# Kernel optimization log

Hardware: AMD Instinct MI355X
Metric: run time of the kernel (lower is better)

## Reference

```python
import jax, jax.numpy as jnp
import numpy as np

NEG = -9e8

def _leaky(x):
    return jax.nn.leaky_relu(x, 0.01)

def _gru(x, h, wih, whh, bih, bhh):
    # torch.nn.GRUCell math
    gi = x @ wih.T + bih
    gh = h @ whh.T + bhh
    ir, iz, inn = jnp.split(gi, 3, axis=-1)
    hr, hz, hn = jnp.split(gh, 3, axis=-1)
    r = jax.nn.sigmoid(ir + hr)
    z = jax.nn.sigmoid(iz + hz)
    n = jnp.tanh(inn + r * hn)
    return (1.0 - z) * n + z * h

def _gather(feat, idx):
    # feat [B,S,F], idx [B,S,K] -> [B,S,K,F]; -1 wraps to last row, masked later (same as torch)
    return jax.vmap(lambda f, i: f[i])(feat, idx)

def setup_inputs() -> dict:
    key = jax.random.key(0)
    ks = jax.random.split(key, 32)
    B, S, K, F_in, E, R = 32, 512, 21, 26, 256, 3
    amino_list = jax.random.uniform(ks[0], (B, S, F_in), dtype=jnp.float32)
    idx = jax.random.randint(ks[1], (B, S, K), 0, S, dtype=jnp.int32)
    pad = jax.random.uniform(ks[2], (B, S, K)) < 0.3
    amino_degree_list = jnp.where(pad, jnp.int32(-1), idx)
    # variable sequence lengths for mask
    lens = jax.random.randint(ks[3], (B,), S // 2, S + 1)
    amino_mask = (jnp.arange(S)[None, :] < lens[:, None]).astype(jnp.float32)
    s = 0.05
    d = dict(
        amino_list=amino_list,
        amino_degree_list=amino_degree_list,
        amino_mask=amino_mask,
        emb_W=jax.random.normal(ks[4], (E, F_in)) * s,
        emb_b=jax.random.normal(ks[5], (E,)) * s,
        neigh_W=jax.random.normal(ks[6], (E, F_in)) * s,
        neigh_b=jax.random.normal(ks[7], (E,)) * s,
        align_W=jax.random.normal(ks[8], (R, 1, 2 * E)) * s,
        align_b=jax.random.normal(ks[9], (R, 1)) * s,
        attend_W=jax.random.normal(ks[10], (R, E, E)) * s,
        attend_b=jax.random.normal(ks[11], (R, E)) * s,
        gru_wih=jax.random.normal(ks[12], (R, 3 * E, E)) * s,
        gru_whh=jax.random.normal(ks[13], (R, 3 * E, E)) * s,
        gru_bih=jax.random.normal(ks[14], (R, 3 * E)) * s,
        gru_bhh=jax.random.normal(ks[15], (R, 3 * E)) * s,
        seq_align_W=jax.random.normal(ks[16], (1, 2 * E)) * s,
        seq_align_b=jax.random.normal(ks[17], (1,)) * s,
        seq_attend_W=jax.random.normal(ks[18], (E, E)) * s,
        seq_attend_b=jax.random.normal(ks[19], (E,)) * s,
        sgru_wih=jax.random.normal(ks[20], (3 * E, E)) * s,
        sgru_whh=jax.random.normal(ks[21], (3 * E, E)) * s,
        sgru_bih=jax.random.normal(ks[22], (3 * E,)) * s,
        sgru_bhh=jax.random.normal(ks[23], (3 * E,)) * s,
    )
    return d

RADIUS = 3
T_STEPS = 2

def reference(amino_list, amino_degree_list, amino_mask,
              emb_W, emb_b, neigh_W, neigh_b,
              align_W, align_b, attend_W, attend_b,
              gru_wih, gru_whh, gru_bih, gru_bhh,
              seq_align_W, seq_align_b, seq_attend_W, seq_attend_b,
              sgru_wih, sgru_whh, sgru_bih, sgru_bhh):
    B, S, _ = amino_list.shape
    E = emb_W.shape[0]
    K = amino_degree_list.shape[-1]

    mask3 = amino_mask[:, :, None]                       # [B,S,1]
    amino_feature = _leaky(amino_list @ emb_W.T + emb_b)  # [B,S,E]

    attend_mask = (amino_degree_list != -1).astype(jnp.float32)[..., None]   # [B,S,K,1]
    softmax_mask = jnp.where(amino_degree_list == -1, NEG, 0.0)[..., None]   # [B,S,K,1]

    # first radius step: neighbors from raw one-hot features via neighbor_fc
    neighbor = _gather(amino_list, amino_degree_list)                 # [B,S,K,F_in]
    neighbor_feature = _leaky(neighbor @ neigh_W.T + neigh_b)         # [B,S,K,E]

    h = amino_feature.reshape(B * S, E)
    activated = None
    for d in range(RADIUS):
        if d == 0:
            nbr = neighbor_feature
            cur = amino_feature
        else:
            nbr = _gather(activated, amino_degree_list)               # [B,S,K,E]
            cur = activated
        cur_exp = jnp.broadcast_to(cur[:, :, None, :], (B, S, K, E))
        feat_align = jnp.concatenate([cur_exp, nbr], axis=-1)         # [B,S,K,2E]
        score = _leaky(feat_align @ align_W[d].T + align_b[d]) + softmax_mask
        attw = jax.nn.softmax(score, axis=-2) * attend_mask           # [B,S,K,1]
        nbr_t = nbr @ attend_W[d].T + attend_b[d]                     # [B,S,K,E]
        context = jax.nn.elu(jnp.sum(attw * nbr_t, axis=-2))          # [B,S,E]
        h = _gru(context.reshape(B * S, E), h, gru_wih[d], gru_whh[d], gru_bih[d], gru_bhh[d])
        activated = jax.nn.relu(h.reshape(B, S, E))

    seq_feature = jnp.sum(activated * mask3, axis=-2)                 # [B,E]
    act_mol = jax.nn.relu(seq_feature)
    seq_softmax_mask = jnp.where(mask3 == 0.0, NEG, 0.0)              # [B,S,1]

    act_seq = act_mol
    for _ in range(T_STEPS):
        mol_exp = jnp.broadcast_to(act_mol[:, None, :], (B, S, E))
        sa = jnp.concatenate([mol_exp, activated], axis=-1)           # [B,S,2E]
        score = _leaky(sa @ seq_align_W.T + seq_align_b) + seq_softmax_mask
        w = jax.nn.softmax(score, axis=-2) * mask3                    # [B,S,1]
        feat_t = activated @ seq_attend_W.T + seq_attend_b            # [B,S,E]
        seq_context = jax.nn.elu(jnp.sum(w * feat_t, axis=-2))        # [B,E]
        seq_feature = _gru(seq_context, seq_feature, sgru_wih, sgru_whh, sgru_bih, sgru_bhh)
        act_seq = jax.nn.relu(seq_feature)
    return act_seq
```

## Files before the change

### kernel.cpp

```cpp
#include <hip/hip_runtime.h>
#include <hip/hip_bf16.h>
#include <math.h>


#define NEGC (-9.0e8f)

typedef __attribute__((ext_vector_type(8))) short bf16x8;
typedef __attribute__((ext_vector_type(4))) float f32x4;

__device__ __forceinline__ ushort f2bf(float x) {
    union { float f; unsigned u; } v; v.f = x;
    unsigned r = v.u + 0x7FFF + ((v.u >> 16) & 1);
    return (ushort)(r >> 16);
}
__device__ __forceinline__ float bf2f(ushort u) {
    union { unsigned u; float f; } v; v.u = ((unsigned)u) << 16;
    return v.f;
}
__device__ __forceinline__ float sigm_fast(float x) {
    return 1.f / (1.f + __expf(-x));
}
__device__ __forceinline__ float tanh_fast(float x) {
    return 1.f - 2.f / (__expf(2.f * x) + 1.f);
}
__device__ __forceinline__ float elu_fast(float x) {
    return x > 0.f ? x : (__expf(x) - 1.f);
}

typedef const __attribute__((address_space(1))) void gvoid_t;
typedef __attribute__((address_space(3))) void lvoid_t;

__global__ __launch_bounds__(256) void cvt3_kernel(
    const float* __restrict__ s0, ushort* __restrict__ d0, int n0,
    const float* __restrict__ s1, ushort* __restrict__ d1, int n1,
    const float* __restrict__ s2, ushort* __restrict__ d2, int n2)
{
    int i = blockIdx.x * 256 + threadIdx.x;
    const float* s; ushort* dst; int l;
    if (i < n0) { s = s0; dst = d0; l = i; }
    else if (i < n0 + n1) { s = s1; dst = d1; l = i - n0; }
    else if (i < n0 + n1 + n2) { s = s2; dst = d2; l = i - n0 - n1; }
    else return;
    float4 v = *reinterpret_cast<const float4*>(s + (size_t)l * 4);
    ushort4 o; o.x = f2bf(v.x); o.y = f2bf(v.y); o.z = f2bf(v.z); o.w = f2bf(v.w);
    *reinterpret_cast<ushort4*>(dst + (size_t)l * 4) = o;
}

__global__ __launch_bounds__(256) void gemm_dual_kernel(
    const ushort* __restrict__ A0, const ushort* __restrict__ W0,
    const float* __restrict__ b0, ushort* __restrict__ C0, int n0t,
    int K,
    const float* __restrict__ dw1, const float* __restrict__ dw2,
    float* __restrict__ dout1, float* __restrict__ dout2)
{
    __shared__ __align__(16) short As[128 * 32];
    __shared__ __align__(16) short Bs[128 * 32];
    int nwg = gridDim.x;
    int q = nwg >> 3;
    int flat = blockIdx.x;
    int sw = (flat & 7) * q + (flat >> 3);
    int bmi = sw / n0t, bni = sw - bmi * n0t;
    const ushort* A = A0; const ushort* W = W0; const float* bias = b0;
    ushort* C = C0; int N = n0t << 7; int bn = bni << 7;
    int bm = bmi << 7;

    int tid = threadIdx.x;
    int lane = tid & 63;
    int w = tid >> 6;
    int wr = w >> 1, wc = w & 1;
    bool dots = (dout1 != nullptr) && (bni == 0);

    f32x4 acc[4][4];
#pragma unroll
    for (int m = 0; m < 4; ++m)
#pragma unroll
        for (int n = 0; n < 4; ++n) acc[m][n] = (f32x4){0.f, 0.f, 0.f, 0.f};
    float p1 = 0.f, p2 = 0.f;

    for (int k0 = 0; k0 < K; k0 += 32) {
#pragma unroll
        for (int i = 0; i < 2; ++i) {
            int e = w * 1024 + i * 512 + lane * 8;
            int r = e >> 5, c = e & 31;
            const ushort* ga = A + (size_t)(bm + r) * K + (k0 + c);
            const ushort* gw = W + (size_t)(bn + r) * K + (k0 + c);
            __builtin_amdgcn_global_load_lds((gvoid_t*)ga, (lvoid_t*)&As[w * 1024 + i * 512], 16, 0, 0);
            __builtin_amdgcn_global_load_lds((gvoid_t*)gw, (lvoid_t*)&Bs[w * 1024 + i * 512], 16, 0, 0);
        }
        __syncthreads();
        bf16x8 af[4], bw[4];
        int ra = wr * 64 + (lane & 15);
        int rb = wc * 64 + (lane & 15);
        int kc = (lane >> 4) * 8;
#pragma unroll
        for (int m = 0; m < 4; ++m)
            af[m] = *reinterpret_cast<const bf16x8*>(&As[(ra + m * 16) * 32 + kc]);
#pragma unroll
        for (int n = 0; n < 4; ++n)
            bw[n] = *reinterpret_cast<const bf16x8*>(&Bs[(rb + n * 16) * 32 + kc]);
#pragma unroll
        for (int m = 0; m < 4; ++m)
#pragma unroll
            for (int n = 0; n < 4; ++n)
                acc[m][n] = __builtin_amdgcn_mfma_f32_16x16x32_bf16(af[m], bw[n], acc[m][n], 0, 0, 0);
        if (dots) {
            int drow = tid >> 1, kh = (tid & 1) << 4;
            const short* ar = &As[drow * 32 + kh];
#pragma unroll
            for (int c = 0; c < 16; ++c) {
                float av = bf2f((ushort)ar[c]);
                p1 = fmaf(av, dw1[k0 + kh + c], p1);
                p2 = fmaf(av, dw2[k0 + kh + c], p2);
            }
        }
        __syncthreads();
    }

    if (dots) {
        p1 += __shfl_xor(p1, 1);
        p2 += __shfl_xor(p2, 1);
        if ((tid & 1) == 0) {
            dout1[bm + (tid >> 1)] = p1;
            dout2[bm + (tid >> 1)] = p2;
        }
    }

    int cr0 = bm + wr * 64 + ((lane >> 4) * 4);
    int cc0 = bn + wc * 64 + (lane & 15);
#pragma unroll
    for (int n = 0; n < 4; ++n) {
        int col = cc0 + n * 16;
        float bv = bias[col];
#pragma unroll
        for (int m = 0; m < 4; ++m) {
            int row0 = cr0 + m * 16;
#pragma unroll
            for (int j = 0; j < 4; ++j) {
                float v = acc[m][n][j] + bv;
                C[(size_t)(row0 + j) * N + col] = f2bf(v);
            }
        }
    }
}

template<bool TAIL>
__global__ __launch_bounds__(256) void gru_fused_kernel(
    const ushort* __restrict__ ctx, const ushort* __restrict__ wih,
    const float* __restrict__ bih, const ushort* __restrict__ whh,
    const float* __restrict__ bhh,
    const ushort* __restrict__ h_in, ushort* __restrict__ h_out,
    ushort* __restrict__ act_bf,
    const float* __restrict__ mask, float* __restrict__ pool_part,
    const float* __restrict__ dsw, float* __restrict__ scor_part, int BS)
{
    __shared__ __align__(16) short lds[16384];
    int flat = blockIdx.x;
    int sw = (flat & 7) * 128 + (flat >> 3);
    int bmi = sw >> 2, ct = sw & 3;
    int bm = bmi << 6;
    int tid = threadIdx.x;
    int lane = tid & 63;
    int w = tid >> 6;
    int wr = w >> 1, wc = w & 1;

    f32x4 acc[6][2][2];
#pragma unroll
    for (int qq = 0; qq < 6; ++qq)
#pragma unroll
        for (int m = 0; m < 2; ++m)
#pragma unroll
            for (int n = 0; n < 2; ++n) acc[qq][m][n] = (f32x4){0.f, 0.f, 0.f, 0.f};

    int srow = tid >> 2, scol = (tid & 3) << 3;
    int ldst = (tid & 0xC0) * 8;
    for (int k0 = 0; k0 < 256; k0 += 32) {
        {
            const ushort* s0 = ctx  + (size_t)(bm + srow) * 256 + k0 + scol;
            const ushort* s1 = h_in + (size_t)(bm + srow) * 256 + k0 + scol;
            __builtin_amdgcn_global_load_lds((gvoid_t*)s0, (lvoid_t*)&lds[ldst], 16, 0, 0);
            __builtin_amdgcn_global_load_lds((gvoid_t*)s1, (lvoid_t*)&lds[2048 + ldst], 16, 0, 0);
#pragma unroll
            for (int qq = 0; qq < 6; ++qq) {
                const ushort* wb = (qq < 3) ? wih : whh;
                int slice = (qq < 3) ? qq : qq - 3;
                const ushort* sv = wb + (size_t)(slice * 256 + ct * 64 + srow) * 256 + k0 + scol;
                __builtin_amdgcn_global_load_lds((gvoid_t*)sv,
                    (lvoid_t*)&lds[(2 + qq) * 2048 + ldst], 16, 0, 0);
            }
        }
        __syncthreads();
        int rl = lane & 15;
        int kc = (lane >> 4) * 8;
        bf16x8 a_c[2], a_h[2];
#pragma unroll
        for (int m = 0; m < 2; ++m) {
            a_c[m] = *reinterpret_cast<const bf16x8*>(&lds[(wr * 32 + m * 16 + rl) * 32 + kc]);
            a_h[m] = *reinterpret_cast<const bf16x8*>(&lds[2048 + (wr * 32 + m * 16 + rl) * 32 + kc]);
        }
#pragma unroll
        for (int qq = 0; qq < 6; ++qq) {
            bf16x8 bw[2];
#pragma unroll
            for (int n = 0; n < 2; ++n)
                bw[n] = *reinterpret_cast<const bf16x8*>(
                    &lds[(2 + qq) * 2048 + (wc * 32 + n * 16 + rl) * 32 + kc]);
#pragma unroll
            for (int m = 0; m < 2; ++m)
#pragma unroll
                for (int n = 0; n < 2; ++n)
                    acc[qq][m][n] = __builtin_amdgcn_mfma_f32_16x16x32_bf16(
                        (qq < 3) ? a_c[m] : a_h[m], bw[n], acc[qq][m][n], 0, 0, 0);
        }
        __syncthreads();
    }

    int rl = lane & 15;
    int r0 = (lane >> 4) * 4;
    float mv[2][4];
    float dswv[2];
    if (TAIL) {
        int b_ = bm >> 9;
        int sbase = bm & 511;
#pragma unroll
        for (int m = 0; m < 2; ++m)
#pragma unroll
            for (int j = 0; j < 4; ++j)
                mv[m][j] = mask[b_ * 512 + sbase + wr * 32 + m * 16 + r0 + j];
#pragma unroll
        for (int n = 0; n < 2; ++n)
            dswv[n] = dsw[ct * 64 + wc * 32 + n * 16 + rl];
    }
    float pm[2] = {0.f, 0.f};
    float ps[2][4] = {{0.f, 0.f, 0.f, 0.f}, {0.f, 0.f, 0.f, 0.f}};

#pragma unroll
    for (int n = 0; n < 2; ++n) {
        int col = ct * 64 + wc * 32 + n * 16 + rl;
        float bir = bih[col], biz = bih[256 + col], bin = bih[512 + col];
        float bhr = bhh[col], bhz = bhh[256 + col], bhn = bhh[512 + col];
#pragma unroll
        for (int m = 0; m < 2; ++m) {
            int row0 = bm + wr * 32 + m * 16 + r0;
#pragma unroll
            for (int j = 0; j < 4; ++j) {
                size_t idx = (size_t)(row0 + j) * 256 + col;
                float r = sigm_fast(acc[0][m][n][j] + bir + acc[3][m][n][j] + bhr);
                float z = sigm_fast(acc[1][m][n][j] + biz + acc[4][m][n][j] + bhz);
                float nn = tanh_fast(acc[2][m][n][j] + bin + r * (acc[5][m][n][j] + bhn));
                float hold = bf2f(h_in[idx]);
                float hh = (1.f - z) * nn + z * hold;
                h_out[idx] = f2bf(hh);
                float a = fmaxf(hh, 0.f);
                act_bf[idx] = f2bf(a);
                if (TAIL) {
                    pm[n] = fmaf(a, mv[m][j], pm[n]);
                    ps[m][j] = fmaf(a, dswv[n], ps[m][j]);
                }
            }
        }
    }

    if (TAIL) {
#pragma unroll
        for (int n = 0; n < 2; ++n) {
            float p = pm[n];
            p += __shfl_xor(p, 16);
            p += __shfl_xor(p, 32);
            if (lane < 16) {
                int b_ = bm >> 9;
                int sc = ((bm & 511) >> 5) + wr;
                int col = ct * 64 + wc * 32 + n * 16 + rl;
                pool_part[((size_t)b_ * 16 + sc) * 256 + col] = p;
            }
        }
#pragma unroll
        for (int m = 0; m < 2; ++m)
#pragma unroll
            for (int j = 0; j < 4; ++j) {
                float p = ps[m][j];
                p += __shfl_xor(p, 1);
                p += __shfl_xor(p, 2);
                p += __shfl_xor(p, 4);
                p += __shfl_xor(p, 8);
                if (rl == 0) {
                    int row = bm + wr * 32 + m * 16 + r0 + j;
                    scor_part[(size_t)(ct * 2 + wc) * BS + row] = p;
                }
            }
    }
}

__global__ __launch_bounds__(256) void embed_kernel(
    const float* __restrict__ amino, const float* __restrict__ embW,
    const float* __restrict__ embB, const float* __restrict__ neighW,
    const float* __restrict__ neighB, const float* __restrict__ alignW,
    ushort* __restrict__ h_bf, ushort* __restrict__ nf_bf,
    float* __restrict__ ca, float* __restrict__ cb)
{
    const int FIN = 26, FPAD = 28, ROWS = 64;
    __shared__ __align__(16) float xs[ROWS][FPAD];
    __shared__ float red1[ROWS][4];
    __shared__ float red2[ROWS][4];
    int tid = threadIdx.x;
    int lane = tid & 63, wv = tid >> 6;
    float wE[FPAD], wN[FPAD];
#pragma unroll
    for (int f = 0; f < FIN; ++f) {
        wE[f] = embW[tid * FIN + f];
        wN[f] = neighW[tid * FIN + f];
    }
    wE[26] = wE[27] = wN[26] = wN[27] = 0.f;
    float b1 = embB[tid], b2 = neighB[tid];
    float w1t = alignW[tid], w2t = alignW[256 + tid];
    int row0 = blockIdx.x * ROWS;
    for (int idx = tid; idx < ROWS * FPAD; idx += 256) {
        int r = idx / FPAD, f = idx - r * FPAD;
        xs[r][f] = (f < FIN) ? amino[(size_t)(row0 + r) * FIN + f] : 0.f;
    }
    __syncthreads();
    for (int r = 0; r < ROWS; ++r) {
        const float4* x4 = reinterpret_cast<const float4*>(xs[r]);
        float a = b1, c = b2;
#pragma unroll
        for (int q = 0; q < 7; ++q) {
            float4 x = x4[q];
            a = fmaf(x.x, wE[4 * q], a);     c = fmaf(x.x, wN[4 * q], c);
            a = fmaf(x.y, wE[4 * q + 1], a); c = fmaf(x.y, wN[4 * q + 1], c);
            a = fmaf(x.z, wE[4 * q + 2], a); c = fmaf(x.z, wN[4 * q + 2], c);
            a = fmaf(x.w, wE[4 * q + 3], a); c = fmaf(x.w, wN[4 * q + 3], c);
        }
        a = a > 0.f ? a : 0.01f * a;
        c = c > 0.f ? c : 0.01f * c;
        size_t idx = (size_t)(row0 + r) * 256 + tid;
        h_bf[idx] = f2bf(a);
        nf_bf[idx] = f2bf(c);
        float p1 = a * w1t, p2 = c * w2t;
#pragma unroll
        for (int off = 32; off > 0; off >>= 1) {
            p1 += __shfl_down(p1, off);
            p2 += __shfl_down(p2, off);
        }
        if (lane == 0) { red1[r][wv] = p1; red2[r][wv] = p2; }
    }
    __syncthreads();
    if (tid < ROWS)
        ca[row0 + tid] = red1[tid][0] + red1[tid][1] + red1[tid][2] + red1[tid][3];
    else if (tid < 2 * ROWS) {
        int r = tid - ROWS;
        cb[row0 + r] = red2[r][0] + red2[r][1] + red2[r][2] + red2[r][3];
    }
}

__global__ __launch_bounds__(256) void attn_kernel(
    const int* __restrict__ deg, const float* __restrict__ ca,
    const float* __restrict__ cbrow, const ushort* __restrict__ act_t,
    const float* __restrict__ alignB, int d,
    ushort* __restrict__ context_bf, int S)
{
    const int KNB = 21;
    int raw = blockIdx.x;
    int bid = (raw & 7) * 512 + (raw >> 3);
    int bs0 = bid * 4;
    int b = bs0 >> 9;
    int tid = threadIdx.x;
    int wv = tid >> 6, lane = tid & 63;
    int bs = bs0 + wv;
    __shared__ float ss[4][KNB];
    __shared__ int   sj[4][KNB];
    if (lane < KNB) {
        int j = deg[bs * KNB + lane];
        float cbv = (j >= 0) ? cbrow[b * S + j] : 0.f;
        float sc = ca[bs] + cbv + alignB[d];
        sc = sc > 0.f ? sc : 0.01f * sc;
        if (j < 0) sc += NEGC;
        sj[wv][lane] = j;
        ss[wv][lane] = sc;
    }
    __syncthreads();
    float mx = -3.4e38f;
#pragma unroll
    for (int k = 0; k < KNB; ++k) mx = fmaxf(mx, ss[wv][k]);
    float se[KNB];
    float sum = 0.f;
#pragma unroll
    for (int k = 0; k < KNB; ++k) { se[k] = __expf(ss[wv][k] - mx); sum += se[k]; }
    float inv = 1.f / sum;
    const ushort* base = act_t + (size_t)b * S * 256 + lane * 4;
    float a0 = 0.f, a1 = 0.f, a2 = 0.f, a3 = 0.f;
#pragma unroll
    for (int k = 0; k < KNB; ++k) {
        int j = sj[wv][k];
        if (j >= 0) {
            ushort4 v = *reinterpret_cast<const ushort4*>(base + (size_t)j * 256);
            float wk = se[k];
            a0 = fmaf(wk, bf2f(v.x), a0);
            a1 = fmaf(wk, bf2f(v.y), a1);
            a2 = fmaf(wk, bf2f(v.z), a2);
            a3 = fmaf(wk, bf2f(v.w), a3);
        }
    }
    ushort4 o;
    o.x = f2bf(elu_fast(a0 * inv));
    o.y = f2bf(elu_fast(a1 * inv));
    o.z = f2bf(elu_fast(a2 * inv));
    o.w = f2bf(elu_fast(a3 * inv));
    *reinterpret_cast<ushort4*>(&context_bf[(size_t)bs * 256 + lane * 4]) = o;
}

__global__ __launch_bounds__(256) void seqpool_sm_kernel(
    const float* __restrict__ partial, const float* __restrict__ saW,
    const float* __restrict__ scor_part, const float* __restrict__ sab,
    const float* __restrict__ mask,
    float* __restrict__ seqfeat, float* __restrict__ wout,
    float* __restrict__ wsumb, int NC, int S, int BS)
{
    int b = blockIdx.x, tid = threadIdx.x;
    int lane = tid & 63, wv = tid >> 6;
    __shared__ float red[4];
    __shared__ float sw[512];
    __shared__ float r1[4], r2[4], r3[4];
    __shared__ float smd;
    float acc = 0.f;
    for (int c = 0; c < NC; ++c)
        acc += partial[((size_t)b * NC + c) * 256 + tid];
    seqfeat[b * 256 + tid] = acc;
    float am = fmaxf(acc, 0.f);
    float p = am * saW[tid];
#pragma unroll
    for (int off = 32; off > 0; off >>= 1) p += __shfl_down(p, off);
    if (lane == 0) red[wv] = p;
    __syncthreads();
    if (tid == 0) smd = red[0] + red[1] + red[2] + red[3];
    __syncthreads();
    float md = smd, sb = sab[0];
    float lm = -3.4e38f;
    for (int s = tid; s < S; s += 256) {
        int row = b * S + s;
        float praw = 0.f;
#pragma unroll
        for (int sl = 0; sl < 8; ++sl) praw += scor_part[(size_t)sl * BS + row];
        float sc = md + praw + sb;
        sc = sc > 0.f ? sc : 0.01f * sc;
        if (mask[row] == 0.f) sc += NEGC;
        sw[s] = sc;
        lm = fmaxf(lm, sc);
    }
#pragma unroll
    for (int off = 32; off > 0; off >>= 1) lm = fmaxf(lm, __shfl_down(lm, off));
    if (lane == 0) r1[wv] = lm;
    __syncthreads();
    float mx = fmaxf(fmaxf(r1[0], r1[1]), fmaxf(r1[2], r1[3]));
    float ls = 0.f, ms = 0.f;
    for (int s = tid; s < S; s += 256) {
        float e = __expf(sw[s] - mx);
        float em = e * mask[b * S + s];
        sw[s] = em;
        ls += e;
        ms += em;
    }
#pragma unroll
    for (int off = 32; off > 0; off >>= 1) {
        ls += __shfl_down(ls, off);
        ms += __shfl_down(ms, off);
    }
    if (lane == 0) { r2[wv] = ls; r3[wv] = ms; }
    __syncthreads();
    float inv = 1.f / (r2[0] + r2[1] + r2[2] + r2[3]);
    if (tid == 0) wsumb[b] = (r3[0] + r3[1] + r3[2] + r3[3]) * inv;
    for (int s = tid; s < S; s += 256)
        wout[b * S + s] = sw[s] * inv;
}

__global__ __launch_bounds__(256) void wpool_kernel(
    const float* __restrict__ w, const ushort* __restrict__ act,
    float* __restrict__ vpart, int S, int CH)
{
    int bc = blockIdx.x;
    int NC = S / CH;
    int b = bc / NC, c = bc - b * NC;
    int tid = threadIdx.x;
    int s0 = c * CH;
    const ushort* ab = act + ((size_t)b * S + s0) * 256;
    const float* wb = w + b * S + s0;
    float acc = 0.f;
    for (int s = 0; s < CH; ++s)
        acc = fmaf(wb[s], bf2f(ab[(size_t)s * 256 + tid]), acc);
    vpart[(size_t)bc * 256 + tid] = acc;
}

__global__ __launch_bounds__(256) void combineV_kernel(
    const float* __restrict__ vpart, float* __restrict__ V, int NC)
{
    int b = blockIdx.x, tid = threadIdx.x;
    float acc = 0.f;
    for (int c = 0; c < NC; ++c)
        acc += vpart[((size_t)b * NC + c) * 256 + tid];
    V[b * 256 + tid] = acc;
}

__global__ __launch_bounds__(256) void sctx_mm_kernel(
    const float* __restrict__ V, const float* __restrict__ seqAttW,
    const float* __restrict__ seqAttB, const float* __restrict__ wsumb,
    float* __restrict__ sctx)
{
    int o = blockIdx.x * 4 + (threadIdx.x >> 6);
    int lane = threadIdx.x & 63;
    int b = o >> 8, col = o & 255;
    const float* vb = V + b * 256;
    const float* wr_ = seqAttW + (size_t)col * 256;
    float p = 0.f;
#pragma unroll
    for (int i = 0; i < 4; ++i) {
        int idx = lane + 64 * i;
        p = fmaf(vb[idx], wr_[idx], p);
    }
#pragma unroll
    for (int off = 32; off > 0; off >>= 1) p += __shfl_down(p, off);
    if (lane == 0)
        sctx[o] = elu_fast(p + wsumb[b] * seqAttB[col]);
}

__global__ __launch_bounds__(256) void sgru_mm_kernel(
    const float* __restrict__ x, const float* __restrict__ hseq,
    const float* __restrict__ wih, const float* __restrict__ whh,
    const float* __restrict__ bih, const float* __restrict__ bhh,
    float* __restrict__ g, int full)
{
    int per_b = full ? 1536 : 768;
    int o = blockIdx.x * 4 + (threadIdx.x >> 6);
    int lane = threadIdx.x & 63;
    int b = o / per_b;
    int j = o - b * per_b;
    if (!full) j += 768;
    const float* src; const float* w; const float* bp; int jj;
    if (j < 768) { src = x + b * 256; w = wih; bp = bih; jj = j; }
    else         { src = hseq + b * 256; w = whh; bp = bhh; jj = j - 768; }
    float p = 0.f;
#pragma unroll
    for (int i = 0; i < 4; ++i) {
        int idx = lane + 64 * i;
        p = fmaf(src[idx], w[(size_t)jj * 256 + idx], p);
    }
#pragma unroll
    for (int off = 32; off > 0; off >>= 1) p += __shfl_down(p, off);
    if (lane == 0) g[b * 1536 + j] = p + bp[jj];
}

__global__ __launch_bounds__(256) void sgru_gate_kernel(
    const float* __restrict__ g, float* __restrict__ hseq, float* __restrict__ out)
{
    int b = blockIdx.x, e = threadIdx.x;
    const float* gr = g + b * 1536;
    float r = sigm_fast(gr[e] + gr[768 + e]);
    float z = sigm_fast(gr[256 + e] + gr[1024 + e]);
    float n = tanh_fast(gr[512 + e] + r * gr[1280 + e]);
    float hv = hseq[b * 256 + e];
    float hn = (1.f - z) * n + z * hv;
    hseq[b * 256 + e] = hn;
    out[b * 256 + e] = fmaxf(hn, 0.f);
}

extern "C" void kernel_launch(void* const* d_in, const int* in_sizes, int n_in,
                              void* d_out, int out_size, void* d_ws, size_t ws_size,
                              hipStream_t stream)
{
    const float* amino   = (const float*)d_in[0];
    const int*   deg     = (const int*)  d_in[1];
    const float* mask    = (const float*)d_in[2];
    const float* embW    = (const float*)d_in[3];
    const float* embB    = (const float*)d_in[4];
    const float* neighW  = (const float*)d_in[5];
    const float* neighB  = (const float*)d_in[6];
    const float* alignW  = (const float*)d_in[7];
    const float* alignB  = (const float*)d_in[8];
    const float* attendW = (const float*)d_in[9];
    const float* attendB = (const float*)d_in[10];
    const float* gruWih  = (const float*)d_in[11];
    const float* gruWhh  = (const float*)d_in[12];
    const float* gruBih  = (const float*)d_in[13];
    const float* gruBhh  = (const float*)d_in[14];
    const float* saW     = (const float*)d_in[15];
    const float* saB     = (const float*)d_in[16];
    const float* seqAttW = (const float*)d_in[17];
    const float* seqAttB = (const float*)d_in[18];
    const float* sWih    = (const float*)d_in[19];
    const float* sWhh    = (const float*)d_in[20];
    const float* sBih    = (const float*)d_in[21];
    const float* sBhh    = (const float*)d_in[22];
    float* out = (float*)d_out;

    const int B = 32, S = 512;
    const int BS = B * S;
    const size_t N1 = (size_t)BS * 256;

    ushort* hA     = (ushort*)d_ws;
    ushort* hB     = hA + N1;
    ushort* act_bf = hB + N1;
    ushort* nb_bf  = act_bf + N1;
    ushort* att_bf = nb_bf + N1;
    ushort* attW_bf = att_bf + N1;
    ushort* wih_bf  = attW_bf + 3 * 256 * 256;
    ushort* whh_bf  = wih_bf + 3 * 768 * 256;
    float* smalls = (float*)(whh_bf + 3 * 768 * 256);
    float* ca    = smalls;
    float* cb    = ca + BS;
    float* wbuf  = cb + BS;
    float* scorp = wbuf + BS;
    float* seqf  = scorp + 8 * BS;
    float* sctx  = seqf + B * 256;
    float* V     = sctx + B * 256;
    float* wsumb = V + B * 256;
    float* g     = wsumb + 256;
    float* part  = g + B * 1536;
    float* vpart = part + B * 16 * 256;

    const int c0 = (3 * 256 * 256) / 4, c1 = (3 * 768 * 256) / 4,
              c2 = (3 * 768 * 256) / 4;
    cvt3_kernel<<<(c0 + c1 + c2 + 255) / 256, 256, 0, stream>>>(
        attendW, attW_bf, c0, gruWih, wih_bf, c1, gruWhh, whh_bf, c2);

    embed_kernel<<<BS / 64, 256, 0, stream>>>(amino, embW, embB, neighW, neighB, alignW,
                                              hA, nb_bf, ca, cb);

    for (int d = 0; d < 3; ++d) {
        const ushort* nbr_bf = (d == 0) ? nb_bf : act_bf;
        const ushort* h_in  = (d & 1) ? hB : hA;
        ushort*       h_out = (d & 1) ? hA : hB;
        gemm_dual_kernel<<<128 * 2, 256, 0, stream>>>(
            nbr_bf, attW_bf + d * 256 * 256, attendB + d * 256, att_bf, 2, 256,
            d == 0 ? (const float*)nullptr : alignW + d * 512,
            d == 0 ? (const float*)nullptr : alignW + d * 512 + 256,
            d == 0 ? (float*)nullptr : ca,
            d == 0 ? (float*)nullptr : cb);
        attn_kernel<<<BS / 4, 256, 0, stream>>>(deg, ca, cb, att_bf, alignB, d, nb_bf, S);
        if (d < 2) {
            gru_fused_kernel<false><<<1024, 256, 0, stream>>>(
                nb_bf, wih_bf + d * 768 * 256, gruBih + d * 768,
                whh_bf + d * 768 * 256, gruBhh + d * 768, h_in, h_out, act_bf,
                (const float*)nullptr, (float*)nullptr,
                (const float*)nullptr, (float*)nullptr, BS);
        } else {
            gru_fused_kernel<true><<<1024, 256, 0, stream>>>(
                nb_bf, wih_bf + d * 768 * 256, gruBih + d * 768,
                whh_bf + d * 768 * 256, gruBhh + d * 768, h_in, h_out, act_bf,
                mask, part, saW + 256, scorp, BS);
        }
    }

    seqpool_sm_kernel<<<B, 256, 0, stream>>>(part, saW, scorp, saB, mask,
                                             seqf, wbuf, wsumb, 16, S, BS);
    wpool_kernel<<<B * 16, 256, 0, stream>>>(wbuf, act_bf, vpart, S, 32);
    combineV_kernel<<<B, 256, 0, stream>>>(vpart, V, 16);
    sctx_mm_kernel<<<B * 256 / 4, 256, 0, stream>>>(V, seqAttW, seqAttB, wsumb, sctx);

    sgru_mm_kernel<<<B * 1536 / 4, 256, 0, stream>>>(sctx, seqf, sWih, sWhh, sBih, sBhh, g, 1);
    sgru_gate_kernel<<<B, 256, 0, stream>>>(g, seqf, out);
    sgru_mm_kernel<<<B * 768 / 4, 256, 0, stream>>>(sctx, seqf, sWih, sWhh, sBih, sBhh, g, 0);
    sgru_gate_kernel<<<B, 256, 0, stream>>>(g, seqf, out);
}
```

Measured before the change: 253.7 us.

## Fold V combine into sctx matmul, branchless neighbor gather, GRU occupancy hint

The combineV kernel is removed and each sctx_mm wavefront now sums the 16 partial V chunks itself, saving one launch at the cost of redundant partial reads across the 256 output columns of each batch. The attention gather loop is made branchless: padded neighbors read row 0 with zero weight, so all loads can be issued without divergence, at the cost of extra loads for padded slots. The GRU fused kernel also gets a launch_bounds occupancy hint of 4 blocks per CU, which may force register spilling.

Measured after the change: 262.8 us. +3.6%, slower.

```diff
diff --git a/kernel.cpp b/kernel.cpp
--- a/kernel.cpp
+++ b/kernel.cpp
@@ -144,7 +144,7 @@
 }
 
 template<bool TAIL>
-__global__ __launch_bounds__(256) void gru_fused_kernel(
+__global__ __launch_bounds__(256, 4) void gru_fused_kernel(
     const ushort* __restrict__ ctx, const ushort* __restrict__ wih,
     const float* __restrict__ bih, const ushort* __restrict__ whh,
     const float* __restrict__ bhh,
@@ -381,23 +381,27 @@
 #pragma unroll
     for (int k = 0; k < KNB; ++k) mx = fmaxf(mx, ss[wv][k]);
     float se[KNB];
+    int js[KNB];
     float sum = 0.f;
 #pragma unroll
-    for (int k = 0; k < KNB; ++k) { se[k] = __expf(ss[wv][k] - mx); sum += se[k]; }
+    for (int k = 0; k < KNB; ++k) {
+        int j = sj[wv][k];
+        float e = __expf(ss[wv][k] - mx);
+        sum += e;
+        se[k] = (j >= 0) ? e : 0.f;
+        js[k] = (j >= 0) ? j : 0;
+    }
     float inv = 1.f / sum;
     const ushort* base = act_t + (size_t)b * S * 256 + lane * 4;
     float a0 = 0.f, a1 = 0.f, a2 = 0.f, a3 = 0.f;
 #pragma unroll
     for (int k = 0; k < KNB; ++k) {
-        int j = sj[wv][k];
-        if (j >= 0) {
-            ushort4 v = *reinterpret_cast<const ushort4*>(base + (size_t)j * 256);
-            float wk = se[k];
-            a0 = fmaf(wk, bf2f(v.x), a0);
-            a1 = fmaf(wk, bf2f(v.y), a1);
-            a2 = fmaf(wk, bf2f(v.z), a2);
-            a3 = fmaf(wk, bf2f(v.w), a3);
-        }
+        ushort4 v = *reinterpret_cast<const ushort4*>(base + (size_t)js[k] * 256);
+        float wk = se[k];
+        a0 = fmaf(wk, bf2f(v.x), a0);
+        a1 = fmaf(wk, bf2f(v.y), a1);
+        a2 = fmaf(wk, bf2f(v.z), a2);
+        a3 = fmaf(wk, bf2f(v.w), a3);
     }
     ushort4 o;
     o.x = f2bf(elu_fast(a0 * inv));
@@ -488,31 +492,23 @@
     vpart[(size_t)bc * 256 + tid] = acc;
 }
 
-__global__ __launch_bounds__(256) void combineV_kernel(
-    const float* __restrict__ vpart, float* __restrict__ V, int NC)
-{
-    int b = blockIdx.x, tid = threadIdx.x;
-    float acc = 0.f;
-    for (int c = 0; c < NC; ++c)
-        acc += vpart[((size_t)b * NC + c) * 256 + tid];
-    V[b * 256 + tid] = acc;
-}
-
 __global__ __launch_bounds__(256) void sctx_mm_kernel(
-    const float* __restrict__ V, const float* __restrict__ seqAttW,
+    const float* __restrict__ vpart, const float* __restrict__ seqAttW,
     const float* __restrict__ seqAttB, const float* __restrict__ wsumb,
-    float* __restrict__ sctx)
+    float* __restrict__ sctx, int NC)
 {
     int o = blockIdx.x * 4 + (threadIdx.x >> 6);
     int lane = threadIdx.x & 63;
     int b = o >> 8, col = o & 255;
-    const float* vb = V + b * 256;
     const float* wr_ = seqAttW + (size_t)col * 256;
     float p = 0.f;
 #pragma unroll
     for (int i = 0; i < 4; ++i) {
         int idx = lane + 64 * i;
-        p = fmaf(vb[idx], wr_[idx], p);
+        float v = 0.f;
+        for (int c = 0; c < 16; ++c)
+            v += vpart[((size_t)b * 16 + c) * 256 + idx];
+        p = fmaf(v, wr_[idx], p);
     }
 #pragma unroll
     for (int off = 32; off > 0; off >>= 1) p += __shfl_down(p, off);
@@ -608,8 +604,7 @@
     float* scorp = wbuf + BS;
     float* seqf  = scorp + 8 * BS;
     float* sctx  = seqf + B * 256;
-    float* V     = sctx + B * 256;
-    float* wsumb = V + B * 256;
+    float* wsumb = sctx + B * 256;
     float* g     = wsumb + 256;
     float* part  = g + B * 1536;
     float* vpart = part + B * 16 * 256;
@@ -650,8 +645,7 @@
     seqpool_sm_kernel<<<B, 256, 0, stream>>>(part, saW, scorp, saB, mask,
                                              seqf, wbuf, wsumb, 16, S, BS);
     wpool_kernel<<<B * 16, 256, 0, stream>>>(wbuf, act_bf, vpart, S, 32);
-    combineV_kernel<<<B, 256, 0, stream>>>(vpart, V, 16);
-    sctx_mm_kernel<<<B * 256 / 4, 256, 0, stream>>>(V, seqAttW, seqAttB, wsumb, sctx);
+    sctx_mm_kernel<<<B * 256 / 4, 256, 0, stream>>>(vpart, seqAttW, seqAttB, wsumb, sctx, 16);
 
     sgru_mm_kernel<<<B * 1536 / 4, 256, 0, stream>>>(sctx, seqf, sWih, sWhh, sBih, sBhh, g, 1);
     sgru_gate_kernel<<<B, 256, 0, stream>>>(g, seqf, out);
```
